# Optimization experiments

Hardware: AMD Instinct MI355X
Metric: run time of the kernel (lower is better)

## Reference

```python
import jax, jax.numpy as jnp
import numpy as np

B, S, E, H, D = 4, 2048, 1024, 16, 64  # batch, seq (n_query==graph_size), embed, heads, qkv_dim


def setup_inputs() -> dict:
    key = jax.random.key(0)
    k1, k2, k3, k4, k5, k6 = jax.random.split(key, 6)
    q = jax.random.normal(k1, (B, S, E), dtype=jnp.float32)
    h = jax.random.normal(k2, (B, S, E), dtype=jnp.float32)
    # mask==True means attention NOT allowed (negative adjacency)
    mask = jax.random.randint(k3, (B, S, S), 0, 2) == 1
    scale = 0.02
    Wq = jax.random.normal(k4, (H * D, E), dtype=jnp.float32) * scale
    Wk = jax.random.normal(k5, (H * D, E), dtype=jnp.float32) * scale
    Wv = jax.random.normal(k6, (H * D, E), dtype=jnp.float32) * scale
    return {"q": q, "h": h, "mask": mask, "Wq": Wq, "Wk": Wk, "Wv": Wv}


def reference(q, h, mask, Wq, Wk, Wv):
    b, sq, e = q.shape
    sk = h.shape[1]
    hd = Wq.shape[0]
    heads = H
    d = hd // heads
    norm = 1.0 / jnp.sqrt(jnp.asarray(d, dtype=q.dtype))
    # Linear(bias=False): y = x @ W^T ; then reshape_by_heads -> (B, H, S, D)
    Q = (q @ Wq.T).reshape(b, sq, heads, d).transpose(0, 2, 1, 3)
    K = (h @ Wk.T).reshape(b, sk, heads, d).transpose(0, 2, 1, 3)
    V = (h @ Wv.T).reshape(b, sk, heads, d).transpose(0, 2, 1, 3)
    compat = norm * jnp.einsum("bhqd,bhkd->bhqk", Q, K)  # (B,H,Sq,Sk)
    compat = jnp.where(mask[:, None, :, :], -jnp.inf, compat)
    attn = jax.nn.softmax(compat, axis=-1)
    out_heads = jnp.einsum("bhqk,bhkd->bhqd", attn, V)
    # transpose(1,2) then concat heads -> (B, Sq, H*D)
    return out_heads.transpose(0, 2, 1, 3).reshape(b, sq, heads * d)
```

## Files before the change

### kernel.cpp

```cpp
#include <hip/hip_runtime.h>
#include <math.h>

#define Bb 4
#define Ss 2048
#define Ee 1024
#define Hh 16
#define Dd 64
#define HD (Hh * Dd)

typedef __attribute__((ext_vector_type(8))) _Float16 f16x8;
typedef __attribute__((ext_vector_type(4))) _Float16 f16x4;
typedef __attribute__((ext_vector_type(4))) float f32x4;

__device__ __forceinline__ void gl_lds16(const void* g, void* l) {
  __builtin_amdgcn_global_load_lds(
      (const __attribute__((address_space(1))) unsigned int*)g,
      (__attribute__((address_space(3))) unsigned int*)l, 16, 0, 0);
}

__global__ __launch_bounds__(256) void cvt_f16(const float* __restrict__ x,
                                               _Float16* __restrict__ y) {
  int i = blockIdx.x * 256 + threadIdx.x;
  float4 v = ((const float4*)x)[i];
  f16x4 o;
  o.x = (_Float16)v.x; o.y = (_Float16)v.y;
  o.z = (_Float16)v.z; o.w = (_Float16)v.w;
  *(f16x4*)(y + 4 * (size_t)i) = o;
}

__global__ __launch_bounds__(256) void mask_pack(const int* __restrict__ mask,
                                                 unsigned long long* __restrict__ pm) {
  int g = blockIdx.x * 256 + threadIdx.x;
  unsigned long long bits = __ballot(mask[g] != 0);
  if ((threadIdx.x & 63) == 0) pm[g >> 6] = bits;
}

__global__ __launch_bounds__(256) void proj_mfma(const _Float16* __restrict__ A,
                                                 const _Float16* __restrict__ W,
                                                 _Float16* __restrict__ Y,
                                                 int doScale) {
  __shared__ _Float16 As[128 * 32];
  __shared__ _Float16 Bs[128 * 32];
  const int tid = threadIdx.x;
  const int wv = tid >> 6, lane = tid & 63;
  const int quad = lane >> 4, l16 = lane & 15;
  const int wr = wv >> 1, wc = wv & 1;
  const int bm = blockIdx.y * 128, bn = blockIdx.x * 128;

  f32x4 acc[4][4];
#pragma unroll
  for (int i = 0; i < 4; ++i)
#pragma unroll
    for (int j = 0; j < 4; ++j) acc[i][j] = (f32x4){0.f, 0.f, 0.f, 0.f};

  for (int k0 = 0; k0 < Ee; k0 += 32) {
    __syncthreads();
#pragma unroll
    for (int i = 0; i < 2; ++i) {
      int cb = wv * 128 + i * 64;
      int c = cb + lane;
      int row = c >> 2, ko = (c & 3) << 3;
      gl_lds16(A + (size_t)(bm + row) * Ee + k0 + ko, (char*)As + (size_t)cb * 16);
      gl_lds16(W + (size_t)(bn + row) * Ee + k0 + ko, (char*)Bs + (size_t)cb * 16);
    }
    __syncthreads();

    f16x8 af[4], bf[4];
#pragma unroll
    for (int i = 0; i < 4; ++i)
      af[i] = *(const f16x8*)&As[(wr * 64 + i * 16 + l16) * 32 + quad * 8];
#pragma unroll
    for (int j = 0; j < 4; ++j)
      bf[j] = *(const f16x8*)&Bs[(wc * 64 + j * 16 + l16) * 32 + quad * 8];
#pragma unroll
    for (int i = 0; i < 4; ++i)
#pragma unroll
      for (int j = 0; j < 4; ++j)
        acc[i][j] = __builtin_amdgcn_mfma_f32_16x16x32_f16(af[i], bf[j], acc[i][j], 0, 0, 0);
  }

  const float s = doScale ? 0.18033688011112042f : 1.0f;
#pragma unroll
  for (int i = 0; i < 4; ++i)
#pragma unroll
    for (int j = 0; j < 4; ++j)
#pragma unroll
      for (int reg = 0; reg < 4; ++reg) {
        int row = bm + wr * 64 + i * 16 + quad * 4 + reg;
        int col = bn + wc * 64 + j * 16 + l16;
        Y[(size_t)row * HD + col] = (_Float16)(acc[i][j][reg] * s);
      }
}

__global__ __launch_bounds__(256) void vtrans(const unsigned short* __restrict__ Vb,
                                              unsigned short* __restrict__ Vt) {
  __shared__ unsigned short T[64][68];
  const int nx = blockIdx.x;
  const int my = blockIdx.y;
  const int m0 = my * 64, n0 = nx * 64;
  const int bsel = m0 >> 11, s0 = m0 & 2047;
  const int tid = threadIdx.x;
  const int r = tid >> 4, c4 = (tid & 15) << 2;
#pragma unroll
  for (int i = 0; i < 4; ++i) {
    ushort4 v = *(const ushort4*)(Vb + (size_t)(m0 + r + i * 16) * HD + n0 + c4);
    T[r + i * 16][c4 + 0] = v.x; T[r + i * 16][c4 + 1] = v.y;
    T[r + i * 16][c4 + 2] = v.z; T[r + i * 16][c4 + 3] = v.w;
  }
  __syncthreads();
#pragma unroll
  for (int i = 0; i < 4; ++i) {
    ushort4 o;
    o.x = T[c4 + 0][r + i * 16]; o.y = T[c4 + 1][r + i * 16];
    o.z = T[c4 + 2][r + i * 16]; o.w = T[c4 + 3][r + i * 16];
    *(ushort4*)(Vt + ((size_t)bsel * HD + n0 + r + i * 16) * Ss + s0 + c4) = o;
  }
}

__global__ __launch_bounds__(256) void attn_mfma2(const _Float16* __restrict__ Qb,
                                                  const _Float16* __restrict__ Kb,
                                                  const _Float16* __restrict__ Vt,
                                                  const unsigned long long* __restrict__ pm,
                                                  float* __restrict__ out) {
  const int bq = blockIdx.x;
  const int h  = blockIdx.y;
  const int b  = blockIdx.z;
  const int tid  = threadIdx.x;
  const int wv   = tid >> 6;
  const int lane = tid & 63;
  const int quad = lane >> 4;
  const int l16  = lane & 15;

  __shared__ _Float16 Ks[64][72];
  __shared__ _Float16 Vs[64][72];

  const int qglob = bq * 64 + wv * 16 + l16;
  const _Float16* qrow = Qb + ((size_t)b * Ss + qglob) * HD + h * Dd;
  const f16x8 qf0 = *(const f16x8*)(qrow + quad * 8);
  const f16x8 qf1 = *(const f16x8*)(qrow + 32 + quad * 8);

  const int r = tid >> 2, c = (tid & 3) << 4;
  const _Float16* kbase = Kb + ((size_t)b * Ss + r) * HD + h * Dd + c;
  const _Float16* vbase = Vt + (((size_t)b * Hh + h) * Dd + r) * Ss + c;

  const unsigned long long* pmrow = pm + ((size_t)b * Ss + qglob) * (Ss >> 6);

  f32x4 O[4] = {{0.f,0.f,0.f,0.f},{0.f,0.f,0.f,0.f},{0.f,0.f,0.f,0.f},{0.f,0.f,0.f,0.f}};
  float lsum = 0.f;

  f16x8 ka = *(const f16x8*)kbase;
  f16x8 kb2 = *(const f16x8*)(kbase + 8);
  f16x8 va = *(const f16x8*)vbase;
  f16x8 vb2 = *(const f16x8*)(vbase + 8);

  for (int kt = 0; kt < Ss; kt += 64) {
    __syncthreads();
    *(f16x8*)&Ks[r][c]     = ka;
    *(f16x8*)&Ks[r][c + 8] = kb2;
    *(f16x8*)&Vs[r][c]     = va;
    *(f16x8*)&Vs[r][c + 8] = vb2;
    {
      const int ktn = (kt + 64) & (Ss - 1);
      ka  = *(const f16x8*)(kbase + (size_t)ktn * HD);
      kb2 = *(const f16x8*)(kbase + (size_t)ktn * HD + 8);
      va  = *(const f16x8*)(vbase + ktn);
      vb2 = *(const f16x8*)(vbase + ktn + 8);
    }
    __syncthreads();

    f32x4 c4[4] = {{0.f,0.f,0.f,0.f},{0.f,0.f,0.f,0.f},{0.f,0.f,0.f,0.f},{0.f,0.f,0.f,0.f}};
#pragma unroll
    for (int sub = 0; sub < 4; ++sub) {
      f16x8 k0 = *(const f16x8*)&Ks[sub * 16 + l16][quad * 8];
      f16x8 k1 = *(const f16x8*)&Ks[sub * 16 + l16][32 + quad * 8];
      c4[sub] = __builtin_amdgcn_mfma_f32_16x16x32_f16(k0, qf0, c4[sub], 0, 0, 0);
      c4[sub] = __builtin_amdgcn_mfma_f32_16x16x32_f16(k1, qf1, c4[sub], 0, 0, 0);
    }

    const unsigned long long mq = pmrow[kt >> 6] >> (quad * 4);
    f16x4 pf[4];
#pragma unroll
    for (int sub = 0; sub < 4; ++sub)
#pragma unroll
      for (int reg = 0; reg < 4; ++reg) {
        float t = ((mq >> (sub * 16 + reg)) & 1ull) ? -3.0e38f : c4[sub][reg];
        float p = __builtin_amdgcn_exp2f(t);
        lsum += p;
        pf[sub][reg] = (_Float16)p;
      }

#pragma unroll
    for (int dt = 0; dt < 4; ++dt)
#pragma unroll
      for (int sub = 0; sub < 4; ++sub) {
        f16x4 vf = *(const f16x4*)&Vs[dt * 16 + l16][sub * 16 + quad * 4];
        O[dt] = __builtin_amdgcn_mfma_f32_16x16x16f16(vf, pf[sub], O[dt], 0, 0, 0);
      }
  }

  lsum += __shfl_xor(lsum, 16, 64);
  lsum += __shfl_xor(lsum, 32, 64);
  const float inv = 1.0f / lsum;

  float* obase = out + ((size_t)b * Ss + qglob) * HD + h * Dd;
#pragma unroll
  for (int dt = 0; dt < 4; ++dt) {
    float4 st;
    st.x = O[dt][0] * inv; st.y = O[dt][1] * inv;
    st.z = O[dt][2] * inv; st.w = O[dt][3] * inv;
    *(float4*)(obase + dt * 16 + quad * 4) = st;
  }
}

extern "C" void kernel_launch(void* const* d_in, const int* in_sizes, int n_in,
                              void* d_out, int out_size, void* d_ws, size_t ws_size,
                              hipStream_t stream) {
  const float* q    = (const float*)d_in[0];
  const float* h    = (const float*)d_in[1];
  const int*   mask = (const int*)d_in[2];
  const float* Wq   = (const float*)d_in[3];
  const float* Wk   = (const float*)d_in[4];
  const float* Wv   = (const float*)d_in[5];
  float* out = (float*)d_out;

  char* ws = (char*)d_ws;
  const size_t MB = 1024 * 1024;
  _Float16* qf  = (_Float16*)(ws);
  _Float16* hf  = (_Float16*)(ws + 16 * MB);
  _Float16* Wqf = (_Float16*)(ws + 32 * MB);
  _Float16* Wkf = (_Float16*)(ws + 34 * MB);
  _Float16* Wvf = (_Float16*)(ws + 36 * MB);
  _Float16* Qb  = (_Float16*)(ws + 38 * MB);
  _Float16* Kb  = (_Float16*)(ws + 54 * MB);
  _Float16* Vb  = (_Float16*)(ws + 70 * MB);
  _Float16* Vt  = (_Float16*)(ws);
  unsigned long long* pm = (unsigned long long*)(ws + 86 * MB);

  const int mat4 = (Bb * Ss * Ee) / 4;
  const int wm4  = (HD * Ee) / 4;

  cvt_f16<<<mat4 / 256, 256, 0, stream>>>(q, qf);
  cvt_f16<<<mat4 / 256, 256, 0, stream>>>(h, hf);
  cvt_f16<<<wm4 / 256, 256, 0, stream>>>(Wq, Wqf);
  cvt_f16<<<wm4 / 256, 256, 0, stream>>>(Wk, Wkf);
  cvt_f16<<<wm4 / 256, 256, 0, stream>>>(Wv, Wvf);

  mask_pack<<<(Bb * Ss * Ss) / 256, 256, 0, stream>>>(mask, pm);

  dim3 pg(HD / 128, (Bb * Ss) / 128);
  proj_mfma<<<pg, 256, 0, stream>>>(qf, Wqf, Qb, 1);
  proj_mfma<<<pg, 256, 0, stream>>>(hf, Wkf, Kb, 0);
  proj_mfma<<<pg, 256, 0, stream>>>(hf, Wvf, Vb, 0);

  vtrans<<<dim3(HD / 64, (Bb * Ss) / 64), 256, 0, stream>>>((const unsigned short*)Vb,
                                                            (unsigned short*)Vt);

  attn_mfma2<<<dim3(Ss / 64, Hh, Bb), 256, 0, stream>>>(Qb, Kb, Vt, pm, out);
}
```

Before: 409.5 us.

## Fuse conversions and QKV projections; double-buffer swizzled LDS GEMM tiles

Result: faster. 398.2 us (-2.8%).

```diff
diff --git a/kernel.cpp b/kernel.cpp
--- a/kernel.cpp
+++ b/kernel.cpp
@@ -18,14 +18,32 @@
       (__attribute__((address_space(3))) unsigned int*)l, 16, 0, 0);
 }
 
-__global__ __launch_bounds__(256) void cvt_f16(const float* __restrict__ x,
-                                               _Float16* __restrict__ y) {
+__global__ __launch_bounds__(256) void cvt_all(const float* __restrict__ q,
+                                               const float* __restrict__ h,
+                                               const float* __restrict__ wq,
+                                               const float* __restrict__ wk,
+                                               const float* __restrict__ wv,
+                                               _Float16* __restrict__ qf,
+                                               _Float16* __restrict__ hf,
+                                               _Float16* __restrict__ wqf,
+                                               _Float16* __restrict__ wkf,
+                                               _Float16* __restrict__ wvf) {
+  const int QH = (Bb * Ss * Ee) / 4;
+  const int WM = (HD * Ee) / 4;
   int i = blockIdx.x * 256 + threadIdx.x;
-  float4 v = ((const float4*)x)[i];
+  const float* src;
+  _Float16* dst;
+  int off;
+  if (i < QH)                { src = q;  dst = qf;  off = i; }
+  else if (i < 2 * QH)       { src = h;  dst = hf;  off = i - QH; }
+  else if (i < 2 * QH + WM)  { src = wq; dst = wqf; off = i - 2 * QH; }
+  else if (i < 2 * QH + 2 * WM) { src = wk; dst = wkf; off = i - 2 * QH - WM; }
+  else                       { src = wv; dst = wvf; off = i - 2 * QH - 2 * WM; }
+  float4 v = ((const float4*)src)[off];
   f16x4 o;
   o.x = (_Float16)v.x; o.y = (_Float16)v.y;
   o.z = (_Float16)v.z; o.w = (_Float16)v.w;
-  *(f16x4*)(y + 4 * (size_t)i) = o;
+  *(f16x4*)(dst + 4 * (size_t)off) = o;
 }
 
 __global__ __launch_bounds__(256) void mask_pack(const int* __restrict__ mask,
@@ -35,17 +53,48 @@
   if ((threadIdx.x & 63) == 0) pm[g >> 6] = bits;
 }
 
-__global__ __launch_bounds__(256) void proj_mfma(const _Float16* __restrict__ A,
-                                                 const _Float16* __restrict__ W,
-                                                 _Float16* __restrict__ Y,
-                                                 int doScale) {
-  __shared__ _Float16 As[128 * 32];
-  __shared__ _Float16 Bs[128 * 32];
+__global__ __launch_bounds__(512) void proj_qkv(const _Float16* __restrict__ qf,
+                                                const _Float16* __restrict__ hf,
+                                                const _Float16* __restrict__ Wqf,
+                                                const _Float16* __restrict__ Wkf,
+                                                const _Float16* __restrict__ Wvf,
+                                                _Float16* __restrict__ Qb,
+                                                _Float16* __restrict__ Kb,
+                                                _Float16* __restrict__ Vb) {
+  __shared__ _Float16 As[2][256 * 64];
+  __shared__ _Float16 Bs[2][128 * 64];
+  const int seg = blockIdx.z;
+  const _Float16* A = (seg == 0) ? qf : hf;
+  const _Float16* W = (seg == 0) ? Wqf : ((seg == 1) ? Wkf : Wvf);
+  _Float16* Y       = (seg == 0) ? Qb  : ((seg == 1) ? Kb  : Vb);
+  const float scale = (seg == 0) ? 0.18033688011112042f : 1.0f;
+
   const int tid = threadIdx.x;
   const int wv = tid >> 6, lane = tid & 63;
   const int quad = lane >> 4, l16 = lane & 15;
   const int wr = wv >> 1, wc = wv & 1;
-  const int bm = blockIdx.y * 128, bn = blockIdx.x * 128;
+  const int bm = blockIdx.y * 256, bn = blockIdx.x * 128;
+
+  auto stage = [&](int buf, int k0) {
+#pragma unroll
+    for (int i = 0; i < 4; ++i) {
+      int cb = wv * 64 + i * 512;
+      int c = cb + lane;
+      int row = c >> 3;
+      int l = (c & 7) ^ (row & 7);
+      gl_lds16(A + (size_t)(bm + row) * Ee + k0 + l * 8,
+               (char*)&As[buf][0] + (size_t)cb * 16);
+    }
+#pragma unroll
+    for (int i = 0; i < 2; ++i) {
+      int cb = wv * 64 + i * 512;
+      int c = cb + lane;
+      int row = c >> 3;
+      int l = (c & 7) ^ (row & 7);
+      gl_lds16(W + (size_t)(bn + row) * Ee + k0 + l * 8,
+               (char*)&Bs[buf][0] + (size_t)cb * 16);
+    }
+  };
 
   f32x4 acc[4][4];
 #pragma unroll
@@ -53,33 +102,40 @@
 #pragma unroll
     for (int j = 0; j < 4; ++j) acc[i][j] = (f32x4){0.f, 0.f, 0.f, 0.f};
 
-  for (int k0 = 0; k0 < Ee; k0 += 32) {
-    __syncthreads();
-#pragma unroll
-    for (int i = 0; i < 2; ++i) {
-      int cb = wv * 128 + i * 64;
-      int c = cb + lane;
-      int row = c >> 2, ko = (c & 3) << 3;
-      gl_lds16(A + (size_t)(bm + row) * Ee + k0 + ko, (char*)As + (size_t)cb * 16);
-      gl_lds16(W + (size_t)(bn + row) * Ee + k0 + ko, (char*)Bs + (size_t)cb * 16);
-    }
-    __syncthreads();
-
-    f16x8 af[4], bf[4];
-#pragma unroll
-    for (int i = 0; i < 4; ++i)
-      af[i] = *(const f16x8*)&As[(wr * 64 + i * 16 + l16) * 32 + quad * 8];
-#pragma unroll
-    for (int j = 0; j < 4; ++j)
-      bf[j] = *(const f16x8*)&Bs[(wc * 64 + j * 16 + l16) * 32 + quad * 8];
-#pragma unroll
-    for (int i = 0; i < 4; ++i)
-#pragma unroll
-      for (int j = 0; j < 4; ++j)
-        acc[i][j] = __builtin_amdgcn_mfma_f32_16x16x32_f16(af[i], bf[j], acc[i][j], 0, 0, 0);
-  }
-
-  const float s = doScale ? 0.18033688011112042f : 1.0f;
+  stage(0, 0);
+  const int NT = Ee / 64;
+  for (int it = 0; it < NT; ++it) {
+    const int buf = it & 1;
+    if (it + 1 < NT) {
+      stage(buf ^ 1, (it + 1) * 64);
+      asm volatile("s_waitcnt vmcnt(6)\n\ts_barrier" ::: "memory");
+    } else {
+      asm volatile("s_waitcnt vmcnt(0)\n\ts_barrier" ::: "memory");
+    }
+#pragma unroll
+    for (int s = 0; s < 2; ++s) {
+      f16x8 af[4], bf[4];
+#pragma unroll
+      for (int i = 0; i < 4; ++i) {
+        int row = wr * 64 + i * 16 + l16;
+        int l = s * 4 + quad;
+        af[i] = *(const f16x8*)&As[buf][row * 64 + ((l ^ (row & 7)) << 3)];
+      }
+#pragma unroll
+      for (int j = 0; j < 4; ++j) {
+        int row = wc * 64 + j * 16 + l16;
+        int l = s * 4 + quad;
+        bf[j] = *(const f16x8*)&Bs[buf][row * 64 + ((l ^ (row & 7)) << 3)];
+      }
+#pragma unroll
+      for (int i = 0; i < 4; ++i)
+#pragma unroll
+        for (int j = 0; j < 4; ++j)
+          acc[i][j] = __builtin_amdgcn_mfma_f32_16x16x32_f16(af[i], bf[j], acc[i][j], 0, 0, 0);
+    }
+    asm volatile("s_barrier" ::: "memory");
+  }
+
 #pragma unroll
   for (int i = 0; i < 4; ++i)
 #pragma unroll
@@ -88,7 +144,7 @@
       for (int reg = 0; reg < 4; ++reg) {
         int row = bm + wr * 64 + i * 16 + quad * 4 + reg;
         int col = bn + wc * 64 + j * 16 + l16;
-        Y[(size_t)row * HD + col] = (_Float16)(acc[i][j][reg] * s);
+        Y[(size_t)row * HD + col] = (_Float16)(acc[i][j][reg] * scale);
       }
 }
 
@@ -236,21 +292,13 @@
   _Float16* Vt  = (_Float16*)(ws);
   unsigned long long* pm = (unsigned long long*)(ws + 86 * MB);
 
-  const int mat4 = (Bb * Ss * Ee) / 4;
-  const int wm4  = (HD * Ee) / 4;
-
-  cvt_f16<<<mat4 / 256, 256, 0, stream>>>(q, qf);
-  cvt_f16<<<mat4 / 256, 256, 0, stream>>>(h, hf);
-  cvt_f16<<<wm4 / 256, 256, 0, stream>>>(Wq, Wqf);
-  cvt_f16<<<wm4 / 256, 256, 0, stream>>>(Wk, Wkf);
-  cvt_f16<<<wm4 / 256, 256, 0, stream>>>(Wv, Wvf);
+  const int total4 = 2 * (Bb * Ss * Ee) / 4 + 3 * (HD * Ee) / 4;
+  cvt_all<<<total4 / 256, 256, 0, stream>>>(q, h, Wq, Wk, Wv, qf, hf, Wqf, Wkf, Wvf);
 
   mask_pack<<<(Bb * Ss * Ss) / 256, 256, 0, stream>>>(mask, pm);
 
-  dim3 pg(HD / 128, (Bb * Ss) / 128);
-  proj_mfma<<<pg, 256, 0, stream>>>(qf, Wqf, Qb, 1);
-  proj_mfma<<<pg, 256, 0, stream>>>(hf, Wkf, Kb, 0);
-  proj_mfma<<<pg, 256, 0, stream>>>(hf, Wvf, Vb, 0);
+  proj_qkv<<<dim3(HD / 128, (Bb * Ss) / 256, 3), 512, 0, stream>>>(
+      qf, hf, Wqf, Wkf, Wvf, Qb, Kb, Vb);
 
   vtrans<<<dim3(HD / 64, (Bb * Ss) / 64), 256, 0, stream>>>((const unsigned short*)Vb,
                                                             (unsigned short*)Vt);
```
